# Performance work log

Hardware: AMD Instinct MI355X
Metric: run time of the kernel (lower is better)

Reference implementation:

```python
import jax, jax.numpy as jnp
import numpy as np

N_NODES = 50000
N_EDGES = 800000
D_IN = 128
N_HEADS = 8
D_OUT = 16  # per head; H*D = 128


def setup_inputs() -> dict:
    key = jax.random.key(0)
    ks = jax.random.split(key, 10)
    HD = N_HEADS * D_OUT
    nfeat = jax.random.normal(ks[0], (N_NODES, D_IN), dtype=jnp.float32)
    efeat = jax.random.normal(ks[1], (N_EDGES, D_IN), dtype=jnp.float32)
    src = jax.random.randint(ks[2], (N_EDGES,), 0, N_NODES, dtype=jnp.int32)
    dst = jax.random.randint(ks[3], (N_EDGES,), 0, N_NODES, dtype=jnp.int32)
    # parameters (Xavier-ish scale)
    W_fc = jax.random.normal(ks[4], (D_IN, HD), dtype=jnp.float32) * 0.05
    attn_l = jax.random.normal(ks[5], (N_HEADS, D_OUT), dtype=jnp.float32) * 0.05
    attn_r = jax.random.normal(ks[6], (N_HEADS, D_OUT), dtype=jnp.float32) * 0.05
    bias = jnp.zeros((HD,), dtype=jnp.float32)
    W_e = jax.random.normal(ks[7], (D_IN, HD), dtype=jnp.float32) * 0.05
    b_e = jnp.zeros((HD,), dtype=jnp.float32)
    return {"nfeat": nfeat, "efeat": efeat, "src": src, "dst": dst,
            "W_fc": W_fc, "attn_l": attn_l, "attn_r": attn_r, "bias": bias,
            "W_e": W_e, "b_e": b_e}


def reference(nfeat, efeat, src, dst, W_fc, attn_l, attn_r, bias, W_e, b_e):
    N = nfeat.shape[0]
    E = src.shape[0]
    H, D = attn_l.shape
    # ---- GATConv (DGL semantics, feat_drop=attn_drop=0, no residual/activation) ----
    hf = nfeat @ W_fc                      # [N, H*D]
    h = hf.reshape(N, H, D)                # [N, H, D]
    el = jnp.einsum('nhd,hd->nh', h, attn_l)   # [N, H]
    er = jnp.einsum('nhd,hd->nh', h, attn_r)   # [N, H]
    # per-edge scores: message src -> dst, softmax over incoming edges of dst
    e = jax.nn.leaky_relu(el[src] + er[dst], negative_slope=0.2)  # [E, H]
    m = jax.ops.segment_max(e, dst, num_segments=N)               # [N, H]
    m = jnp.where(jnp.isfinite(m), m, jnp.zeros_like(m))          # empty segments -> 0
    ex = jnp.exp(e - m[dst])                                      # [E, H]
    denom = jax.ops.segment_sum(ex, dst, num_segments=N)          # [N, H]
    a = ex / denom[dst]                                           # [E, H]
    agg = jax.ops.segment_sum(a[:, :, None] * h[src], dst, num_segments=N)  # [N, H, D]
    gat = agg.reshape(N, H * D) + bias                            # flatten(1) + bias
    # ---- skip term: fc(nfeat) / (in_degree + 1) ----
    ones = jnp.ones((E,), dtype=nfeat.dtype)
    indeg = jax.ops.segment_sum(ones, dst, num_segments=N)        # [N]
    sfeat = hf / (indeg + 1.0)[:, None]
    out = gat + sfeat
    # ---- econv: edge feature mean aggregation (copy_e + mean over in-edges) ----
    ef = efeat @ W_e + b_e                                        # [E, H*D]
    esum = jax.ops.segment_sum(ef, dst, num_segments=N)           # [N, H*D]
    h_e = esum / jnp.maximum(indeg, 1.0)[:, None]                 # zero-deg -> 0
    return out + h_e
```

## Files before the change

### kernel.cpp

```cpp
#include <hip/hip_runtime.h>
#include <math.h>

#define NN 50000
#define NE 800000
#define HD 128
#define NH 8
#define DO 16
#define NEG_BIG -3.0e38f

__global__ void init_kernel(int* __restrict__ indeg) {
    int i = blockIdx.x * blockDim.x + threadIdx.x;
    if (i < NN) indeg[i] = 0;
}

__global__ void count_deg_kernel(const int* __restrict__ dst, int* __restrict__ indeg) {
    int e = blockIdx.x * blockDim.x + threadIdx.x;
    if (e < NE) atomicAdd(&indeg[dst[e]], 1);
}

__global__ __launch_bounds__(1024) void scan_kernel(const int* __restrict__ indeg,
                                                    int* __restrict__ offsets,
                                                    int* __restrict__ cursor) {
    __shared__ int part[1024];
    const int t = threadIdx.x;
    const int CH = (NN + 1023) / 1024;
    int b = t * CH, e = min(b + CH, NN);
    int s = 0;
    for (int i = b; i < e; ++i) s += indeg[i];
    part[t] = s;
    __syncthreads();
    for (int off = 1; off < 1024; off <<= 1) {
        int v = (t >= off) ? part[t - off] : 0;
        __syncthreads();
        part[t] += v;
        __syncthreads();
    }
    int base = (t == 0) ? 0 : part[t - 1];
    for (int i = b; i < e; ++i) {
        offsets[i] = base;
        cursor[i] = base;
        base += indeg[i];
    }
    if (t == 1023) offsets[NN] = base;
}

__global__ void scatter_kernel(const int* __restrict__ src, const int* __restrict__ dst,
                               int* __restrict__ cursor, int2* __restrict__ sorted) {
    int e = blockIdx.x * blockDim.x + threadIdx.x;
    if (e < NE) {
        int d = dst[e];
        int pos = atomicAdd(&cursor[d], 1);
        sorted[pos] = make_int2(src[e], e);
    }
}

template<bool FUSE_ATTN, bool ADD>
__global__ __launch_bounds__(256) void gemm128_kernel(
    const float* __restrict__ A, const float* __restrict__ W,
    float* __restrict__ out,
    const float* __restrict__ attn_l, const float* __restrict__ attn_r,
    float* __restrict__ el, float* __restrict__ er)
{
    __shared__ float sW[HD * HD];
    __shared__ float sA[32 * HD];
    const int tid = threadIdx.x;
    float4* sWv = (float4*)sW;
    float4* sAv = (float4*)sA;
    const float4* Wv = (const float4*)W;
    for (int j = tid; j < HD * 32; j += 256) sWv[j] = Wv[j];

    const int tc = tid & 15;
    const int tr = tid >> 4;
    const int ra = 2 * tr, rb = ra + 1;
    const int sx = (tr & 3) << 3;
    const float4* Av = (const float4*)A;

    for (int row0 = blockIdx.x * 32; row0 < NN; row0 += gridDim.x * 32) {
        __syncthreads();
#pragma unroll
        for (int j = 0; j < 4; ++j) {
            int f = tid + j * 256;
            int rr = f >> 5, c4 = f & 31;
            int gr = row0 + rr;
            float4 v = make_float4(0.f, 0.f, 0.f, 0.f);
            if (gr < NN) v = Av[(size_t)gr * 32 + c4];
            sAv[rr * 32 + (c4 ^ (((rr >> 1) & 3) << 1))] = v;
        }
        __syncthreads();

        float4 a00 = make_float4(0.f,0.f,0.f,0.f), a01 = a00, a10 = a00, a11 = a00;
#pragma unroll 4
        for (int k = 0; k < HD; ++k) {
            float4 w0 = sWv[k * 32 + 2 * tc];
            float4 w1 = sWv[k * 32 + 2 * tc + 1];
            float xa = sA[ra * HD + (k ^ sx)];
            float xb = sA[rb * HD + (k ^ sx)];
            a00.x = fmaf(xa, w0.x, a00.x); a00.y = fmaf(xa, w0.y, a00.y);
            a00.z = fmaf(xa, w0.z, a00.z); a00.w = fmaf(xa, w0.w, a00.w);
            a01.x = fmaf(xa, w1.x, a01.x); a01.y = fmaf(xa, w1.y, a01.y);
            a01.z = fmaf(xa, w1.z, a01.z); a01.w = fmaf(xa, w1.w, a01.w);
            a10.x = fmaf(xb, w0.x, a10.x); a10.y = fmaf(xb, w0.y, a10.y);
            a10.z = fmaf(xb, w0.z, a10.z); a10.w = fmaf(xb, w0.w, a10.w);
            a11.x = fmaf(xb, w1.x, a11.x); a11.y = fmaf(xb, w1.y, a11.y);
            a11.z = fmaf(xb, w1.z, a11.z); a11.w = fmaf(xb, w1.w, a11.w);
        }

        const int ga = row0 + ra, gb = row0 + rb;

        if (FUSE_ATTN) {
            const int hh = tc >> 1;
            const int db = (tc & 1) << 3;
            const float* al  = attn_l + hh * DO + db;
            const float* arr = attn_r + hh * DO + db;
            float sl_a = a00.x*al[0] + a00.y*al[1] + a00.z*al[2] + a00.w*al[3]
                       + a01.x*al[4] + a01.y*al[5] + a01.z*al[6] + a01.w*al[7];
            float sr_a = a00.x*arr[0] + a00.y*arr[1] + a00.z*arr[2] + a00.w*arr[3]
                       + a01.x*arr[4] + a01.y*arr[5] + a01.z*arr[6] + a01.w*arr[7];
            float sl_b = a10.x*al[0] + a10.y*al[1] + a10.z*al[2] + a10.w*al[3]
                       + a11.x*al[4] + a11.y*al[5] + a11.z*al[6] + a11.w*al[7];
            float sr_b = a10.x*arr[0] + a10.y*arr[1] + a10.z*arr[2] + a10.w*arr[3]
                       + a11.x*arr[4] + a11.y*arr[5] + a11.z*arr[6] + a11.w*arr[7];
            sl_a += __shfl_xor(sl_a, 1);  sr_a += __shfl_xor(sr_a, 1);
            sl_b += __shfl_xor(sl_b, 1);  sr_b += __shfl_xor(sr_b, 1);
            if (!(tc & 1)) {
                if (ga < NN) { el[ga * NH + hh] = sl_a; er[ga * NH + hh] = sr_a; }
                if (gb < NN) { el[gb * NH + hh] = sl_b; er[gb * NH + hh] = sr_b; }
            }
        }

        float4* outv = (float4*)out;
        if (ga < NN) {
            size_t b = (size_t)ga * 32 + 2 * tc;
            if (ADD) {
                float4 p0 = outv[b], p1 = outv[b + 1];
                p0.x += a00.x; p0.y += a00.y; p0.z += a00.z; p0.w += a00.w;
                p1.x += a01.x; p1.y += a01.y; p1.z += a01.z; p1.w += a01.w;
                outv[b] = p0; outv[b + 1] = p1;
            } else {
                outv[b] = a00; outv[b + 1] = a01;
            }
        }
        if (gb < NN) {
            size_t b = (size_t)gb * 32 + 2 * tc;
            if (ADD) {
                float4 p0 = outv[b], p1 = outv[b + 1];
                p0.x += a10.x; p0.y += a10.y; p0.z += a10.z; p0.w += a10.w;
                p1.x += a11.x; p1.y += a11.y; p1.z += a11.z; p1.w += a11.w;
                outv[b] = p0; outv[b + 1] = p1;
            } else {
                outv[b] = a10; outv[b + 1] = a11;
            }
        }
    }
}

__global__ __launch_bounds__(256) void node_kernel(
    const int2* __restrict__ sorted, const int* __restrict__ offsets,
    const float* __restrict__ hf, const float* __restrict__ efeat,
    const float* __restrict__ el, const float* __restrict__ er,
    const float* __restrict__ bias, const float* __restrict__ b_e,
    float* __restrict__ out, float* __restrict__ eaggs)
{
    int wv   = threadIdx.x >> 6;
    int lane = threadIdx.x & 63;
    int node = blockIdx.x * 4 + wv;
    if (node >= NN) return;
    int beg = offsets[node];
    int end = offsets[node + 1];

    int h = lane & 7;
    float er_h = er[node * NH + h];
    float m = NEG_BIG, ssum = 0.0f;
    for (int i = beg + (lane >> 3); i < end; i += 8) {
        int s = sorted[i].x;
        float x = el[s * NH + h] + er_h;
        x = x > 0.0f ? x : 0.2f * x;
        if (x > m) { ssum = ssum * __expf(m - x) + 1.0f; m = x; }
        else        ssum += __expf(x - m);
    }
#pragma unroll
    for (int off = 8; off < 64; off <<= 1) {
        float mo = __shfl_xor(m, off);
        float so = __shfl_xor(ssum, off);
        float mn = fmaxf(m, mo);
        ssum = ssum * __expf(m - mn) + so * __expf(mo - mn);
        m = mn;
    }
    float r = ssum > 0.0f ? 1.0f / ssum : 0.0f;

    int h1 = lane >> 4;
    int h2 = h1 + 4;
    float m1 = __shfl(m, h1), r1 = __shfl(r, h1);
    float m2 = __shfl(m, h2), r2 = __shfl(r, h2);
    float er1 = er[node * NH + h1];
    float er2 = er[node * NH + h2];

    float acc0 = 0.0f, acc1 = 0.0f, ea0 = 0.0f, ea1 = 0.0f;
#pragma unroll 4
    for (int i = beg; i < end; ++i) {
        int2 se = sorted[i];
        int s = se.x;
        size_t eb = (size_t)se.y * HD;
        float x1 = el[s * NH + h1] + er1; x1 = x1 > 0.0f ? x1 : 0.2f * x1;
        float x2 = el[s * NH + h2] + er2; x2 = x2 > 0.0f ? x2 : 0.2f * x2;
        float w1 = __expf(x1 - m1) * r1;
        float w2 = __expf(x2 - m2) * r2;
        acc0 += w1 * hf[(size_t)s * HD + lane];
        acc1 += w2 * hf[(size_t)s * HD + lane + 64];
        ea0 += efeat[eb + lane];
        ea1 += efeat[eb + lane + 64];
    }

    float deg  = (float)(end - beg);
    float rdeg = 1.0f / fmaxf(deg, 1.0f);
    float rskip = 1.0f / (deg + 1.0f);
    float bsel = deg > 0.0f ? 1.0f : 0.0f;
    size_t o = (size_t)node * HD;
    out[o + lane]      = acc0 + bias[lane]      + hf[o + lane]      * rskip + bsel * b_e[lane];
    out[o + lane + 64] = acc1 + bias[lane + 64] + hf[o + lane + 64] * rskip + bsel * b_e[lane + 64];
    eaggs[o + lane]      = ea0 * rdeg;
    eaggs[o + lane + 64] = ea1 * rdeg;
}

extern "C" void kernel_launch(void* const* d_in, const int* in_sizes, int n_in,
                              void* d_out, int out_size, void* d_ws, size_t ws_size,
                              hipStream_t stream) {
    const float* nfeat  = (const float*)d_in[0];
    const float* efeat  = (const float*)d_in[1];
    const int*   src    = (const int*)d_in[2];
    const int*   dst    = (const int*)d_in[3];
    const float* W_fc   = (const float*)d_in[4];
    const float* attn_l = (const float*)d_in[5];
    const float* attn_r = (const float*)d_in[6];
    const float* bias   = (const float*)d_in[7];
    const float* W_e    = (const float*)d_in[8];
    const float* b_e    = (const float*)d_in[9];
    float* out = (float*)d_out;

    float* ws = (float*)d_ws;
    size_t o = 0;
    float* hf      = ws + o; o += (size_t)NN * HD;
    float* el      = ws + o; o += (size_t)NN * NH;
    float* er      = ws + o; o += (size_t)NN * NH;
    int*   indeg   = (int*)(ws + o); o += NN;
    int*   offsets = (int*)(ws + o); o += NN + 1;
    int*   cursor  = (int*)(ws + o); o += NN;
    o = (o + 1) & ~(size_t)1;
    int2*  sorted  = (int2*)(ws + o); o += (size_t)NE * 2;
    float* eaggs   = ws + o; o += (size_t)NN * HD;

    init_kernel<<<(NN + 255) / 256, 256, 0, stream>>>(indeg);
    count_deg_kernel<<<(NE + 255) / 256, 256, 0, stream>>>(dst, indeg);
    scan_kernel<<<1, 1024, 0, stream>>>(indeg, offsets, cursor);
    scatter_kernel<<<(NE + 255) / 256, 256, 0, stream>>>(src, dst, cursor, sorted);

    gemm128_kernel<true, false><<<(NN + 31) / 32, 256, 0, stream>>>(
        nfeat, W_fc, hf, attn_l, attn_r, el, er);

    node_kernel<<<(NN + 3) / 4, 256, 0, stream>>>(sorted, offsets, hf, efeat,
                                                  el, er, bias, b_e, out, eaggs);

    gemm128_kernel<false, true><<<(NN + 31) / 32, 256, 0, stream>>>(
        eaggs, W_e, out, nullptr, nullptr, nullptr, nullptr);
}
```

Before: 916.6 us.

## Retile GEMM to 64-row blocks with chunked W, vectorize node gather over edges

The GEMM now handles 64 rows per block, keeps a 4x2 float4 accumulator tile per thread and streams W through shared memory in 32-row chunks. This cuts shared memory per block (64 KB W plus 16 KB A before) so several blocks can be resident, and it adds a launch-bounds occupancy hint. The node kernel processes four edges at once per wavefront using float4 loads of hf and efeat, then reduces across edge slots with shuffles. This aims to raise memory-level parallelism in the dominant gather, at the cost of masked tail iterations and an extra cross-lane reduction.

```diff
diff --git a/kernel.cpp b/kernel.cpp
--- a/kernel.cpp
+++ b/kernel.cpp
@@ -7,6 +7,15 @@
 #define NH 8
 #define DO 16
 #define NEG_BIG -3.0e38f
+
+__device__ inline void fma4(float4& a, float s, const float4& b) {
+    a.x = fmaf(s, b.x, a.x); a.y = fmaf(s, b.y, a.y);
+    a.z = fmaf(s, b.z, a.z); a.w = fmaf(s, b.w, a.w);
+}
+__device__ inline void red4(float4& a, int off) {
+    a.x += __shfl_xor(a.x, off); a.y += __shfl_xor(a.y, off);
+    a.z += __shfl_xor(a.z, off); a.w += __shfl_xor(a.w, off);
+}
 
 __global__ void init_kernel(int* __restrict__ indeg) {
     int i = blockIdx.x * blockDim.x + threadIdx.x;
@@ -55,100 +64,101 @@
 }
 
 template<bool FUSE_ATTN, bool ADD>
-__global__ __launch_bounds__(256) void gemm128_kernel(
+__global__ __launch_bounds__(256, 3) void gemm64_kernel(
     const float* __restrict__ A, const float* __restrict__ W,
     float* __restrict__ out,
     const float* __restrict__ attn_l, const float* __restrict__ attn_r,
     float* __restrict__ el, float* __restrict__ er)
 {
-    __shared__ float sW[HD * HD];
-    __shared__ float sA[32 * HD];
+    __shared__ float sA[64 * HD];
+    __shared__ float sW[32 * HD];
     const int tid = threadIdx.x;
-    float4* sWv = (float4*)sW;
-    float4* sAv = (float4*)sA;
-    const float4* Wv = (const float4*)W;
-    for (int j = tid; j < HD * 32; j += 256) sWv[j] = Wv[j];
-
     const int tc = tid & 15;
     const int tr = tid >> 4;
-    const int ra = 2 * tr, rb = ra + 1;
-    const int sx = (tr & 3) << 3;
+    const int row0 = blockIdx.x * 64;
+
     const float4* Av = (const float4*)A;
-
-    for (int row0 = blockIdx.x * 32; row0 < NN; row0 += gridDim.x * 32) {
+    float4* sAv = (float4*)sA;
+#pragma unroll
+    for (int j = 0; j < 8; ++j) {
+        int f = tid + j * 256;
+        int r = f >> 5, g = f & 31;
+        int gr = row0 + r;
+        float4 v = make_float4(0.f, 0.f, 0.f, 0.f);
+        if (gr < NN) v = Av[(size_t)gr * 32 + g];
+        sAv[r * 32 + (g ^ ((r & 3) << 1))] = v;
+    }
+
+    float4 acc[4][2];
+#pragma unroll
+    for (int rj = 0; rj < 4; ++rj) {
+        acc[rj][0] = make_float4(0.f, 0.f, 0.f, 0.f);
+        acc[rj][1] = make_float4(0.f, 0.f, 0.f, 0.f);
+    }
+
+    const float4* Wv = (const float4*)W;
+    float4* sWv = (float4*)sW;
+    for (int kc = 0; kc < 4; ++kc) {
         __syncthreads();
 #pragma unroll
         for (int j = 0; j < 4; ++j) {
             int f = tid + j * 256;
-            int rr = f >> 5, c4 = f & 31;
-            int gr = row0 + rr;
-            float4 v = make_float4(0.f, 0.f, 0.f, 0.f);
-            if (gr < NN) v = Av[(size_t)gr * 32 + c4];
-            sAv[rr * 32 + (c4 ^ (((rr >> 1) & 3) << 1))] = v;
+            sWv[f] = Wv[(size_t)(kc * 32 + (f >> 5)) * 32 + (f & 31)];
         }
         __syncthreads();
-
-        float4 a00 = make_float4(0.f,0.f,0.f,0.f), a01 = a00, a10 = a00, a11 = a00;
-#pragma unroll 4
-        for (int k = 0; k < HD; ++k) {
-            float4 w0 = sWv[k * 32 + 2 * tc];
-            float4 w1 = sWv[k * 32 + 2 * tc + 1];
-            float xa = sA[ra * HD + (k ^ sx)];
-            float xb = sA[rb * HD + (k ^ sx)];
-            a00.x = fmaf(xa, w0.x, a00.x); a00.y = fmaf(xa, w0.y, a00.y);
-            a00.z = fmaf(xa, w0.z, a00.z); a00.w = fmaf(xa, w0.w, a00.w);
-            a01.x = fmaf(xa, w1.x, a01.x); a01.y = fmaf(xa, w1.y, a01.y);
-            a01.z = fmaf(xa, w1.z, a01.z); a01.w = fmaf(xa, w1.w, a01.w);
-            a10.x = fmaf(xb, w0.x, a10.x); a10.y = fmaf(xb, w0.y, a10.y);
-            a10.z = fmaf(xb, w0.z, a10.z); a10.w = fmaf(xb, w0.w, a10.w);
-            a11.x = fmaf(xb, w1.x, a11.x); a11.y = fmaf(xb, w1.y, a11.y);
-            a11.z = fmaf(xb, w1.z, a11.z); a11.w = fmaf(xb, w1.w, a11.w);
-        }
-
-        const int ga = row0 + ra, gb = row0 + rb;
-
-        if (FUSE_ATTN) {
-            const int hh = tc >> 1;
-            const int db = (tc & 1) << 3;
-            const float* al  = attn_l + hh * DO + db;
-            const float* arr = attn_r + hh * DO + db;
-            float sl_a = a00.x*al[0] + a00.y*al[1] + a00.z*al[2] + a00.w*al[3]
-                       + a01.x*al[4] + a01.y*al[5] + a01.z*al[6] + a01.w*al[7];
-            float sr_a = a00.x*arr[0] + a00.y*arr[1] + a00.z*arr[2] + a00.w*arr[3]
-                       + a01.x*arr[4] + a01.y*arr[5] + a01.z*arr[6] + a01.w*arr[7];
-            float sl_b = a10.x*al[0] + a10.y*al[1] + a10.z*al[2] + a10.w*al[3]
-                       + a11.x*al[4] + a11.y*al[5] + a11.z*al[6] + a11.w*al[7];
-            float sr_b = a10.x*arr[0] + a10.y*arr[1] + a10.z*arr[2] + a10.w*arr[3]
-                       + a11.x*arr[4] + a11.y*arr[5] + a11.z*arr[6] + a11.w*arr[7];
-            sl_a += __shfl_xor(sl_a, 1);  sr_a += __shfl_xor(sr_a, 1);
-            sl_b += __shfl_xor(sl_b, 1);  sr_b += __shfl_xor(sr_b, 1);
-            if (!(tc & 1)) {
-                if (ga < NN) { el[ga * NH + hh] = sl_a; er[ga * NH + hh] = sr_a; }
-                if (gb < NN) { el[gb * NH + hh] = sl_b; er[gb * NH + hh] = sr_b; }
+#pragma unroll 8
+        for (int kk = 0; kk < 32; ++kk) {
+            float4 w0 = sWv[kk * 32 + tc];
+            float4 w1 = sWv[kk * 32 + 16 + tc];
+            int k = kc * 32 + kk;
+#pragma unroll
+            for (int rj = 0; rj < 4; ++rj) {
+                int r = tr + rj * 16;
+                float a = sA[r * HD + (k ^ ((r & 3) << 3))];
+                fma4(acc[rj][0], a, w0);
+                fma4(acc[rj][1], a, w1);
             }
         }
-
-        float4* outv = (float4*)out;
-        if (ga < NN) {
-            size_t b = (size_t)ga * 32 + 2 * tc;
-            if (ADD) {
-                float4 p0 = outv[b], p1 = outv[b + 1];
-                p0.x += a00.x; p0.y += a00.y; p0.z += a00.z; p0.w += a00.w;
-                p1.x += a01.x; p1.y += a01.y; p1.z += a01.z; p1.w += a01.w;
-                outv[b] = p0; outv[b + 1] = p1;
-            } else {
-                outv[b] = a00; outv[b + 1] = a01;
+    }
+
+    if (FUSE_ATTN) {
+        const int h1 = tc >> 2, q = tc & 3;
+        float4 al0 = ((const float4*)attn_l)[h1 * 4 + q];
+        float4 ar0 = ((const float4*)attn_r)[h1 * 4 + q];
+        float4 al1 = ((const float4*)attn_l)[(h1 + 4) * 4 + q];
+        float4 ar1 = ((const float4*)attn_r)[(h1 + 4) * 4 + q];
+#pragma unroll
+        for (int rj = 0; rj < 4; ++rj) {
+            float sl0 = acc[rj][0].x * al0.x + acc[rj][0].y * al0.y + acc[rj][0].z * al0.z + acc[rj][0].w * al0.w;
+            float sr0 = acc[rj][0].x * ar0.x + acc[rj][0].y * ar0.y + acc[rj][0].z * ar0.z + acc[rj][0].w * ar0.w;
+            float sl1 = acc[rj][1].x * al1.x + acc[rj][1].y * al1.y + acc[rj][1].z * al1.z + acc[rj][1].w * al1.w;
+            float sr1 = acc[rj][1].x * ar1.x + acc[rj][1].y * ar1.y + acc[rj][1].z * ar1.z + acc[rj][1].w * ar1.w;
+            sl0 += __shfl_xor(sl0, 1); sl0 += __shfl_xor(sl0, 2);
+            sr0 += __shfl_xor(sr0, 1); sr0 += __shfl_xor(sr0, 2);
+            sl1 += __shfl_xor(sl1, 1); sl1 += __shfl_xor(sl1, 2);
+            sr1 += __shfl_xor(sr1, 1); sr1 += __shfl_xor(sr1, 2);
+            int gr = row0 + tr + rj * 16;
+            if (q == 0 && gr < NN) {
+                el[gr * NH + h1]     = sl0;  er[gr * NH + h1]     = sr0;
+                el[gr * NH + h1 + 4] = sl1;  er[gr * NH + h1 + 4] = sr1;
             }
         }
-        if (gb < NN) {
-            size_t b = (size_t)gb * 32 + 2 * tc;
+    }
+
+    float4* outv = (float4*)out;
+#pragma unroll
+    for (int rj = 0; rj < 4; ++rj) {
+        int gr = row0 + tr + rj * 16;
+        if (gr < NN) {
+            size_t b = (size_t)gr * 32;
             if (ADD) {
-                float4 p0 = outv[b], p1 = outv[b + 1];
-                p0.x += a10.x; p0.y += a10.y; p0.z += a10.z; p0.w += a10.w;
-                p1.x += a11.x; p1.y += a11.y; p1.z += a11.z; p1.w += a11.w;
-                outv[b] = p0; outv[b + 1] = p1;
+                float4 p0 = outv[b + tc], p1 = outv[b + 16 + tc];
+                p0.x += acc[rj][0].x; p0.y += acc[rj][0].y; p0.z += acc[rj][0].z; p0.w += acc[rj][0].w;
+                p1.x += acc[rj][1].x; p1.y += acc[rj][1].y; p1.z += acc[rj][1].z; p1.w += acc[rj][1].w;
+                outv[b + tc] = p0; outv[b + 16 + tc] = p1;
             } else {
-                outv[b] = a10; outv[b + 1] = a11;
+                outv[b + tc] = acc[rj][0];
+                outv[b + 16 + tc] = acc[rj][1];
             }
         }
     }
@@ -188,38 +198,71 @@
     }
     float r = ssum > 0.0f ? 1.0f / ssum : 0.0f;
 
-    int h1 = lane >> 4;
-    int h2 = h1 + 4;
+    const int eslot = lane >> 4;
+    const int cg    = lane & 15;
+    const int h1 = cg >> 2, h2 = h1 + 4;
     float m1 = __shfl(m, h1), r1 = __shfl(r, h1);
     float m2 = __shfl(m, h2), r2 = __shfl(r, h2);
     float er1 = er[node * NH + h1];
     float er2 = er[node * NH + h2];
 
-    float acc0 = 0.0f, acc1 = 0.0f, ea0 = 0.0f, ea1 = 0.0f;
-#pragma unroll 4
-    for (int i = beg; i < end; ++i) {
-        int2 se = sorted[i];
+    const float4* hfv = (const float4*)hf;
+    const float4* efv = (const float4*)efeat;
+    float4 acc0 = make_float4(0.f,0.f,0.f,0.f), acc1 = acc0, ea0 = acc0, ea1 = acc0;
+
+#pragma unroll 2
+    for (int i0 = beg; i0 < end; i0 += 4) {
+        int i = i0 + eslot;
+        bool valid = i < end;
+        int2 se = sorted[valid ? i : beg];
         int s = se.x;
-        size_t eb = (size_t)se.y * HD;
+        size_t eb = (size_t)se.y * 32;
         float x1 = el[s * NH + h1] + er1; x1 = x1 > 0.0f ? x1 : 0.2f * x1;
         float x2 = el[s * NH + h2] + er2; x2 = x2 > 0.0f ? x2 : 0.2f * x2;
-        float w1 = __expf(x1 - m1) * r1;
-        float w2 = __expf(x2 - m2) * r2;
-        acc0 += w1 * hf[(size_t)s * HD + lane];
-        acc1 += w2 * hf[(size_t)s * HD + lane + 64];
-        ea0 += efeat[eb + lane];
-        ea1 += efeat[eb + lane + 64];
-    }
-
-    float deg  = (float)(end - beg);
-    float rdeg = 1.0f / fmaxf(deg, 1.0f);
-    float rskip = 1.0f / (deg + 1.0f);
-    float bsel = deg > 0.0f ? 1.0f : 0.0f;
-    size_t o = (size_t)node * HD;
-    out[o + lane]      = acc0 + bias[lane]      + hf[o + lane]      * rskip + bsel * b_e[lane];
-    out[o + lane + 64] = acc1 + bias[lane + 64] + hf[o + lane + 64] * rskip + bsel * b_e[lane + 64];
-    eaggs[o + lane]      = ea0 * rdeg;
-    eaggs[o + lane + 64] = ea1 * rdeg;
+        float vm = valid ? 1.0f : 0.0f;
+        float w1 = __expf(x1 - m1) * r1 * vm;
+        float w2 = __expf(x2 - m2) * r2 * vm;
+        float4 hv0 = hfv[(size_t)s * 32 + cg];
+        float4 hv1 = hfv[(size_t)s * 32 + 16 + cg];
+        float4 ev0 = efv[eb + cg];
+        float4 ev1 = efv[eb + 16 + cg];
+        fma4(acc0, w1, hv0);
+        fma4(acc1, w2, hv1);
+        fma4(ea0, vm, ev0);
+        fma4(ea1, vm, ev1);
+    }
+
+#pragma unroll
+    for (int off = 16; off < 64; off <<= 1) {
+        red4(acc0, off); red4(acc1, off);
+        red4(ea0, off);  red4(ea1, off);
+    }
+
+    if (eslot == 0) {
+        float deg   = (float)(end - beg);
+        float rdeg  = 1.0f / fmaxf(deg, 1.0f);
+        float rskip = 1.0f / (deg + 1.0f);
+        float bsel  = deg > 0.0f ? 1.0f : 0.0f;
+        size_t ob = (size_t)node * 32;
+        float4 b0  = ((const float4*)bias)[cg],     b1  = ((const float4*)bias)[16 + cg];
+        float4 be0 = ((const float4*)b_e)[cg],      be1 = ((const float4*)b_e)[16 + cg];
+        float4 hf0 = hfv[ob + cg],                  hf1 = hfv[ob + 16 + cg];
+        float4 o0, o1, g0, g1;
+        o0.x = acc0.x + b0.x + hf0.x * rskip + bsel * be0.x;
+        o0.y = acc0.y + b0.y + hf0.y * rskip + bsel * be0.y;
+        o0.z = acc0.z + b0.z + hf0.z * rskip + bsel * be0.z;
+        o0.w = acc0.w + b0.w + hf0.w * rskip + bsel * be0.w;
+        o1.x = acc1.x + b1.x + hf1.x * rskip + bsel * be1.x;
+        o1.y = acc1.y + b1.y + hf1.y * rskip + bsel * be1.y;
+        o1.z = acc1.z + b1.z + hf1.z * rskip + bsel * be1.z;
+        o1.w = acc1.w + b1.w + hf1.w * rskip + bsel * be1.w;
+        g0.x = ea0.x * rdeg; g0.y = ea0.y * rdeg; g0.z = ea0.z * rdeg; g0.w = ea0.w * rdeg;
+        g1.x = ea1.x * rdeg; g1.y = ea1.y * rdeg; g1.z = ea1.z * rdeg; g1.w = ea1.w * rdeg;
+        ((float4*)out)[ob + cg]        = o0;
+        ((float4*)out)[ob + 16 + cg]   = o1;
+        ((float4*)eaggs)[ob + cg]      = g0;
+        ((float4*)eaggs)[ob + 16 + cg] = g1;
+    }
 }
 
 extern "C" void kernel_launch(void* const* d_in, const int* in_sizes, int n_in,
@@ -254,12 +297,12 @@
     scan_kernel<<<1, 1024, 0, stream>>>(indeg, offsets, cursor);
     scatter_kernel<<<(NE + 255) / 256, 256, 0, stream>>>(src, dst, cursor, sorted);
 
-    gemm128_kernel<true, false><<<(NN + 31) / 32, 256, 0, stream>>>(
+    gemm64_kernel<true, false><<<(NN + 63) / 64, 256, 0, stream>>>(
         nfeat, W_fc, hf, attn_l, attn_r, el, er);
 
     node_kernel<<<(NN + 3) / 4, 256, 0, stream>>>(sorted, offsets, hf, efeat,
                                                   el, er, bias, b_e, out, eaggs);
 
-    gemm128_kernel<false, true><<<(NN + 31) / 32, 256, 0, stream>>>(
+    gemm64_kernel<false, true><<<(NN + 63) / 64, 256, 0, stream>>>(
         eaggs, W_e, out, nullptr, nullptr, nullptr, nullptr);
 }
```

Result: faster. 881.1 us (-3.9%).
